# Performance work log

Hardware: AMD Instinct MI355X
Metric: run time of the kernel (lower is better)

## Reference

```python
import jax, jax.numpy as jnp
import numpy as np

WEIGHT_BIT = 8
ACT_BIT = 8
EPS = 1e-8

def ste_round(v):
    # straight-through estimator round (matches torch ste_round in QAT)
    return v + jax.lax.stop_gradient(jnp.round(v) - v)

def setup_inputs() -> dict:
    key = jax.random.key(0)
    k1, k2, k3, k4 = jax.random.split(key, 4)
    B, D_IN, D_OUT = 8192, 4096, 4096
    x = jax.random.normal(k1, (B, D_IN), dtype=jnp.float32)
    act_scaling_factor = jax.random.uniform(k2, (1,), dtype=jnp.float32, minval=0.01, maxval=0.05)
    W = jax.random.normal(k3, (D_OUT, D_IN), dtype=jnp.float32) * 0.02
    b = jax.random.normal(k4, (D_OUT,), dtype=jnp.float32) * 0.02
    return {"x": x, "act_scaling_factor": act_scaling_factor, "W": W, "b": b}

def reference(x, act_scaling_factor, W, b):
    n_w = 2 ** (WEIGHT_BIT - 1) - 1  # 127
    # ---- QuantLinear: symmetric per-channel weight quantization ----
    w_absmax = jnp.maximum(jnp.abs(W.min(axis=1)), jnp.abs(W.max(axis=1)))  # [out]
    fc_sf = jnp.maximum(w_absmax, EPS) / n_w  # weight scaling factor, [out]
    w_int = jnp.clip(ste_round(W / fc_sf[:, None]), -n_w - 1, n_w)
    bias_sf = fc_sf * act_scaling_factor  # [out] (act_sf is scalar-shaped [1])
    b_int = ste_round(b / bias_sf)
    x_int = x / act_scaling_factor
    out = (jnp.matmul(x_int, w_int.T) + b_int) * bias_sf  # [B, out]
    # ---- ReLU ----
    out = jax.nn.relu(out)
    # ---- QuantAct, asymmetric per-tensor requantization ----
    levels = 2 ** ACT_BIT - 1  # 255
    x_min = jnp.minimum(out.min(), 0.0)
    x_max = jnp.maximum(out.max(), 0.0)
    act_sf_new = jnp.maximum(x_max - x_min, EPS) / levels  # scalar
    zp = jnp.round(-x_min / act_sf_new)
    x_q = jnp.clip(ste_round(out / act_sf_new) + zp, 0.0, float(levels))
    x_out = (x_q - zp) * act_sf_new
    return (x_out, fc_sf, jnp.reshape(act_sf_new, (1,)))
```

## Files before the change

kernel.cpp:

```cpp
#include <hip/hip_runtime.h>
#include <hip/hip_bf16.h>
#include <stdint.h>

#define B_DIM 8192
#define IN_DIM 4096
#define OUT_DIM 4096

typedef __attribute__((ext_vector_type(8))) short s16x8;
typedef __attribute__((ext_vector_type(4))) float f32x4;

__device__ __forceinline__ unsigned short f2bf_rn(float f) {
    unsigned int u = __float_as_uint(f);
    u = (u + 0x7FFFu + ((u >> 16) & 1u)) >> 16;
    return (unsigned short)u;
}

__device__ __forceinline__ void async16(unsigned short* l, const unsigned short* g) {
    __builtin_amdgcn_global_load_lds(
        (const __attribute__((address_space(1))) void*)g,
        (__attribute__((address_space(3))) void*)l, 16, 0, 0);
}

__global__ __launch_bounds__(256) void quant_w(
    const float* __restrict__ W, const float* __restrict__ b,
    const float* __restrict__ act_sf, unsigned short* __restrict__ wq,
    float* __restrict__ fc_sf_out, float* __restrict__ bb,
    float* __restrict__ gmax)
{
    int o = blockIdx.x;
    int t = threadIdx.x;
    const float4* Wr = (const float4*)(W + (size_t)o * IN_DIM);
    float4 v[4];
    float amax = 0.f;
#pragma unroll
    for (int j = 0; j < 4; ++j) {
        v[j] = Wr[t + j * 256];
        amax = fmaxf(amax, fmaxf(fmaxf(fabsf(v[j].x), fabsf(v[j].y)),
                                 fmaxf(fabsf(v[j].z), fabsf(v[j].w))));
    }
#pragma unroll
    for (int off = 32; off > 0; off >>= 1)
        amax = fmaxf(amax, __shfl_down(amax, off, 64));
    __shared__ float red[4];
    if ((t & 63) == 0) red[t >> 6] = amax;
    __syncthreads();
    float wmax = fmaxf(fmaxf(red[0], red[1]), fmaxf(red[2], red[3]));
    float sf = fmaxf(wmax, 1e-8f) / 127.0f;

    unsigned short* wr = wq + (size_t)o * IN_DIM;
#pragma unroll
    for (int j = 0; j < 4; ++j) {
        ushort4 q;
        q.x = f2bf_rn(fminf(fmaxf(rintf(v[j].x / sf), -128.f), 127.f));
        q.y = f2bf_rn(fminf(fmaxf(rintf(v[j].y / sf), -128.f), 127.f));
        q.z = f2bf_rn(fminf(fmaxf(rintf(v[j].z / sf), -128.f), 127.f));
        q.w = f2bf_rn(fminf(fmaxf(rintf(v[j].w / sf), -128.f), 127.f));
        ((ushort4*)wr)[t + j * 256] = q;
    }
    if (t == 0) {
        fc_sf_out[o] = sf;
        float bsf = sf * act_sf[0];
        float bi = rintf(b[o] / bsf);
        bb[o] = bi * bsf;
        if (o == 0) gmax[0] = 0.f;
    }
}

__global__ __launch_bounds__(256) void cvt_x(const float* __restrict__ x,
                                             unsigned short* __restrict__ xq)
{
    size_t i = ((size_t)blockIdx.x * 256 + threadIdx.x) * 8;
#pragma unroll
    for (int j = 0; j < 2; ++j) {
        float4 v = *(const float4*)(x + i + j * 4);
        ushort4 q;
        q.x = f2bf_rn(v.x); q.y = f2bf_rn(v.y);
        q.z = f2bf_rn(v.z); q.w = f2bf_rn(v.w);
        *(ushort4*)(xq + i + j * 4) = q;
    }
}

__global__ __launch_bounds__(256) void gemm_bt(
    const unsigned short* __restrict__ A, const unsigned short* __restrict__ Bw,
    const float* __restrict__ fc_sf, const float* __restrict__ bb,
    float* __restrict__ C, float* __restrict__ gmax)
{
    __shared__ unsigned short sA[128 * 32];
    __shared__ unsigned short sB[128 * 32];
    __shared__ float redm[4];

    int t = threadIdx.x;
    int bn = blockIdx.x & 31;
    int bm = blockIdx.x >> 5;
    int lane = t & 63;
    int w = t >> 6;
    int quad = lane >> 4;
    int l16 = lane & 15;
    int m0 = bm * 128, n0 = bn * 128;
    int wm = (w & 1) * 64, wn = (w >> 1) * 64;

    int r0 = t >> 2;
    int gc = (t & 3) ^ ((r0 & 3) ^ ((r0 >> 2) & 1));
    const unsigned short* gA0 = A + (size_t)(m0 + r0) * IN_DIM + gc * 8;
    const unsigned short* gA1 = A + (size_t)(m0 + 64 + r0) * IN_DIM + gc * 8;
    const unsigned short* gB0 = Bw + (size_t)(n0 + r0) * IN_DIM + gc * 8;
    const unsigned short* gB1 = Bw + (size_t)(n0 + 64 + r0) * IN_DIM + gc * 8;
    unsigned short* lA0 = sA + t * 8;
    unsigned short* lA1 = sA + (t + 256) * 8;
    unsigned short* lB0 = sB + t * 8;
    unsigned short* lB1 = sB + (t + 256) * 8;

    int swzl = (l16 & 3) ^ ((l16 >> 2) & 1);
    const unsigned short* pa = sA + (wm + l16) * 32 + ((quad ^ swzl) * 8);
    const unsigned short* pb = sB + (wn + l16) * 32 + ((quad ^ swzl) * 8);

    f32x4 acc[4][4];
#pragma unroll
    for (int mi = 0; mi < 4; ++mi)
#pragma unroll
        for (int ni = 0; ni < 4; ++ni)
            acc[mi][ni] = (f32x4){0.f, 0.f, 0.f, 0.f};

    for (int kk = 0; kk < IN_DIM; kk += 32) {
        __syncthreads();
        async16(lA0, gA0 + kk);
        async16(lA1, gA1 + kk);
        async16(lB0, gB0 + kk);
        async16(lB1, gB1 + kk);
        asm volatile("s_waitcnt vmcnt(0)" ::: "memory");
        __syncthreads();

        s16x8 af[4], bf[4];
#pragma unroll
        for (int i = 0; i < 4; ++i) af[i] = *(const s16x8*)(pa + i * 16 * 32);
#pragma unroll
        for (int i = 0; i < 4; ++i) bf[i] = *(const s16x8*)(pb + i * 16 * 32);
#pragma unroll
        for (int mi = 0; mi < 4; ++mi)
#pragma unroll
            for (int ni = 0; ni < 4; ++ni)
                acc[mi][ni] = __builtin_amdgcn_mfma_f32_16x16x32_bf16(
                    af[mi], bf[ni], acc[mi][ni], 0, 0, 0);
    }

    float tmax = 0.f;
#pragma unroll
    for (int ni = 0; ni < 4; ++ni) {
        int col = n0 + wn + ni * 16 + l16;
        float s = fc_sf[col];
        float bbv = bb[col];
#pragma unroll
        for (int mi = 0; mi < 4; ++mi) {
            int rowb = m0 + wm + mi * 16 + quad * 4;
#pragma unroll
            for (int r = 0; r < 4; ++r) {
                float vv = acc[mi][ni][r] * s + bbv;
                vv = fmaxf(vv, 0.f);
                tmax = fmaxf(tmax, vv);
                C[(size_t)(rowb + r) * OUT_DIM + col] = vv;
            }
        }
    }
#pragma unroll
    for (int off = 32; off > 0; off >>= 1)
        tmax = fmaxf(tmax, __shfl_down(tmax, off, 64));
    if (lane == 0) redm[w] = tmax;
    __syncthreads();
    if (t == 0) {
        float bmax = fmaxf(fmaxf(redm[0], redm[1]), fmaxf(redm[2], redm[3]));
        atomicMax((int*)gmax, __float_as_int(bmax));
    }
}

__global__ __launch_bounds__(256) void requant(float* __restrict__ C,
    const float* __restrict__ gmax, float* __restrict__ sf_out)
{
    float sf = fmaxf(gmax[0], 1e-8f) / 255.0f;
    size_t i = ((size_t)blockIdx.x * 256 + threadIdx.x) * 8;
#pragma unroll
    for (int j = 0; j < 2; ++j) {
        float4 v = *(const float4*)(C + i + j * 4);
        v.x = fminf(rintf(v.x / sf), 255.f) * sf;
        v.y = fminf(rintf(v.y / sf), 255.f) * sf;
        v.z = fminf(rintf(v.z / sf), 255.f) * sf;
        v.w = fminf(rintf(v.w / sf), 255.f) * sf;
        *(float4*)(C + i + j * 4) = v;
    }
    if (i == 0) sf_out[0] = sf;
}

extern "C" void kernel_launch(void* const* d_in, const int* in_sizes, int n_in,
                              void* d_out, int out_size, void* d_ws, size_t ws_size,
                              hipStream_t stream)
{
    const float* x      = (const float*)d_in[0];
    const float* act_sf = (const float*)d_in[1];
    const float* W      = (const float*)d_in[2];
    const float* b      = (const float*)d_in[3];

    float* out        = (float*)d_out;
    float* fc_sf_out  = out + (size_t)B_DIM * OUT_DIM;
    float* act_sf_out = fc_sf_out + OUT_DIM;

    char* ws = (char*)d_ws;
    float* bb   = (float*)ws;
    float* gmax = (float*)(ws + 16384);
    unsigned short* xq = (unsigned short*)(ws + 32768);
    unsigned short* wq = xq + (size_t)B_DIM * IN_DIM;

    quant_w<<<OUT_DIM, 256, 0, stream>>>(W, b, act_sf, wq, fc_sf_out, bb, gmax);
    cvt_x<<<(B_DIM * IN_DIM) / 2048, 256, 0, stream>>>(x, xq);
    gemm_bt<<<(B_DIM / 128) * (OUT_DIM / 128), 256, 0, stream>>>(
        xq, wq, fc_sf_out, bb, out, gmax);
    requant<<<(B_DIM * OUT_DIM) / 2048, 256, 0, stream>>>(out, gmax, act_sf_out);
}
```

Before: 639.9 us.

## Double GEMM K-tile to 64, merge prep kernels, widen requant per-thread work

The GEMM K-step grows from 32 to 64, with an 8-way XOR swizzle for the wider LDS rows, so each barrier pair now feeds 32 MFMAs instead of 16. The weight quantization and x-to-bf16 conversion kernels become one launch that branches on block index. The requant kernel now processes 16 floats per thread with half as many blocks. This cuts sync overhead and launch count in exchange for twice the LDS per block, which may lower occupancy, and there is still no double buffering.

Result: no change. 632.2 us (-1.2%).

```diff
diff --git a/kernel.cpp b/kernel.cpp
--- a/kernel.cpp
+++ b/kernel.cpp
@@ -21,62 +21,61 @@
         (__attribute__((address_space(3))) void*)l, 16, 0, 0);
 }
 
-__global__ __launch_bounds__(256) void quant_w(
+__global__ __launch_bounds__(256) void prep(
     const float* __restrict__ W, const float* __restrict__ b,
-    const float* __restrict__ act_sf, unsigned short* __restrict__ wq,
+    const float* __restrict__ act_sf, const float* __restrict__ x,
+    unsigned short* __restrict__ wq, unsigned short* __restrict__ xq,
     float* __restrict__ fc_sf_out, float* __restrict__ bb,
     float* __restrict__ gmax)
 {
-    int o = blockIdx.x;
+    __shared__ float red[4];
     int t = threadIdx.x;
-    const float4* Wr = (const float4*)(W + (size_t)o * IN_DIM);
-    float4 v[4];
-    float amax = 0.f;
-#pragma unroll
-    for (int j = 0; j < 4; ++j) {
-        v[j] = Wr[t + j * 256];
-        amax = fmaxf(amax, fmaxf(fmaxf(fabsf(v[j].x), fabsf(v[j].y)),
-                                 fmaxf(fabsf(v[j].z), fabsf(v[j].w))));
-    }
-#pragma unroll
-    for (int off = 32; off > 0; off >>= 1)
-        amax = fmaxf(amax, __shfl_down(amax, off, 64));
-    __shared__ float red[4];
-    if ((t & 63) == 0) red[t >> 6] = amax;
-    __syncthreads();
-    float wmax = fmaxf(fmaxf(red[0], red[1]), fmaxf(red[2], red[3]));
-    float sf = fmaxf(wmax, 1e-8f) / 127.0f;
-
-    unsigned short* wr = wq + (size_t)o * IN_DIM;
-#pragma unroll
-    for (int j = 0; j < 4; ++j) {
-        ushort4 q;
-        q.x = f2bf_rn(fminf(fmaxf(rintf(v[j].x / sf), -128.f), 127.f));
-        q.y = f2bf_rn(fminf(fmaxf(rintf(v[j].y / sf), -128.f), 127.f));
-        q.z = f2bf_rn(fminf(fmaxf(rintf(v[j].z / sf), -128.f), 127.f));
-        q.w = f2bf_rn(fminf(fmaxf(rintf(v[j].w / sf), -128.f), 127.f));
-        ((ushort4*)wr)[t + j * 256] = q;
-    }
-    if (t == 0) {
-        fc_sf_out[o] = sf;
-        float bsf = sf * act_sf[0];
-        float bi = rintf(b[o] / bsf);
-        bb[o] = bi * bsf;
-        if (o == 0) gmax[0] = 0.f;
-    }
-}
-
-__global__ __launch_bounds__(256) void cvt_x(const float* __restrict__ x,
-                                             unsigned short* __restrict__ xq)
-{
-    size_t i = ((size_t)blockIdx.x * 256 + threadIdx.x) * 8;
-#pragma unroll
-    for (int j = 0; j < 2; ++j) {
-        float4 v = *(const float4*)(x + i + j * 4);
-        ushort4 q;
-        q.x = f2bf_rn(v.x); q.y = f2bf_rn(v.y);
-        q.z = f2bf_rn(v.z); q.w = f2bf_rn(v.w);
-        *(ushort4*)(xq + i + j * 4) = q;
+    if (blockIdx.x < OUT_DIM) {
+        int o = blockIdx.x;
+        const float4* Wr = (const float4*)(W + (size_t)o * IN_DIM);
+        float4 v[4];
+        float amax = 0.f;
+#pragma unroll
+        for (int j = 0; j < 4; ++j) {
+            v[j] = Wr[t + j * 256];
+            amax = fmaxf(amax, fmaxf(fmaxf(fabsf(v[j].x), fabsf(v[j].y)),
+                                     fmaxf(fabsf(v[j].z), fabsf(v[j].w))));
+        }
+#pragma unroll
+        for (int off = 32; off > 0; off >>= 1)
+            amax = fmaxf(amax, __shfl_down(amax, off, 64));
+        if ((t & 63) == 0) red[t >> 6] = amax;
+        __syncthreads();
+        float wmax = fmaxf(fmaxf(red[0], red[1]), fmaxf(red[2], red[3]));
+        float sf = fmaxf(wmax, 1e-8f) / 127.0f;
+
+        unsigned short* wr = wq + (size_t)o * IN_DIM;
+#pragma unroll
+        for (int j = 0; j < 4; ++j) {
+            ushort4 q;
+            q.x = f2bf_rn(fminf(fmaxf(rintf(v[j].x / sf), -128.f), 127.f));
+            q.y = f2bf_rn(fminf(fmaxf(rintf(v[j].y / sf), -128.f), 127.f));
+            q.z = f2bf_rn(fminf(fmaxf(rintf(v[j].z / sf), -128.f), 127.f));
+            q.w = f2bf_rn(fminf(fmaxf(rintf(v[j].w / sf), -128.f), 127.f));
+            ((ushort4*)wr)[t + j * 256] = q;
+        }
+        if (t == 0) {
+            fc_sf_out[o] = sf;
+            float bsf = sf * act_sf[0];
+            float bi = rintf(b[o] / bsf);
+            bb[o] = bi * bsf;
+            if (o == 0) gmax[0] = 0.f;
+        }
+    } else {
+        size_t i = ((size_t)(blockIdx.x - OUT_DIM) * 256 + t) * 8;
+#pragma unroll
+        for (int j = 0; j < 2; ++j) {
+            float4 v = *(const float4*)(x + i + j * 4);
+            ushort4 q;
+            q.x = f2bf_rn(v.x); q.y = f2bf_rn(v.y);
+            q.z = f2bf_rn(v.z); q.w = f2bf_rn(v.w);
+            *(ushort4*)(xq + i + j * 4) = q;
+        }
     }
 }
 
@@ -85,8 +84,8 @@
     const float* __restrict__ fc_sf, const float* __restrict__ bb,
     float* __restrict__ C, float* __restrict__ gmax)
 {
-    __shared__ unsigned short sA[128 * 32];
-    __shared__ unsigned short sB[128 * 32];
+    __shared__ unsigned short sA[128 * 64];
+    __shared__ unsigned short sB[128 * 64];
     __shared__ float redm[4];
 
     int t = threadIdx.x;
@@ -99,20 +98,28 @@
     int m0 = bm * 128, n0 = bn * 128;
     int wm = (w & 1) * 64, wn = (w >> 1) * 64;
 
-    int r0 = t >> 2;
-    int gc = (t & 3) ^ ((r0 & 3) ^ ((r0 >> 2) & 1));
-    const unsigned short* gA0 = A + (size_t)(m0 + r0) * IN_DIM + gc * 8;
-    const unsigned short* gA1 = A + (size_t)(m0 + 64 + r0) * IN_DIM + gc * 8;
-    const unsigned short* gB0 = Bw + (size_t)(n0 + r0) * IN_DIM + gc * 8;
-    const unsigned short* gB1 = Bw + (size_t)(n0 + 64 + r0) * IN_DIM + gc * 8;
-    unsigned short* lA0 = sA + t * 8;
-    unsigned short* lA1 = sA + (t + 256) * 8;
-    unsigned short* lB0 = sB + t * 8;
-    unsigned short* lB1 = sB + (t + 256) * 8;
-
-    int swzl = (l16 & 3) ^ ((l16 >> 2) & 1);
-    const unsigned short* pa = sA + (wm + l16) * 32 + ((quad ^ swzl) * 8);
-    const unsigned short* pb = sB + (wn + l16) * 32 + ((quad ^ swzl) * 8);
+    int r0 = t >> 3;
+    int gc = (t & 7) ^ (r0 & 7);
+    const unsigned short* gA[4];
+    const unsigned short* gB[4];
+    unsigned short* lA[4];
+    unsigned short* lB[4];
+#pragma unroll
+    for (int j = 0; j < 4; ++j) {
+        gA[j] = A + (size_t)(m0 + j * 32 + r0) * IN_DIM + gc * 8;
+        gB[j] = Bw + (size_t)(n0 + j * 32 + r0) * IN_DIM + gc * 8;
+        lA[j] = sA + (j * 256 + t) * 8;
+        lB[j] = sB + (j * 256 + t) * 8;
+    }
+
+    int swzl = l16 & 7;
+    const unsigned short* pa[2];
+    const unsigned short* pb[2];
+#pragma unroll
+    for (int h = 0; h < 2; ++h) {
+        pa[h] = sA + (wm + l16) * 64 + ((4 * h + quad) ^ swzl) * 8;
+        pb[h] = sB + (wn + l16) * 64 + ((4 * h + quad) ^ swzl) * 8;
+    }
 
     f32x4 acc[4][4];
 #pragma unroll
@@ -121,26 +128,30 @@
         for (int ni = 0; ni < 4; ++ni)
             acc[mi][ni] = (f32x4){0.f, 0.f, 0.f, 0.f};
 
-    for (int kk = 0; kk < IN_DIM; kk += 32) {
+    for (int kk = 0; kk < IN_DIM; kk += 64) {
         __syncthreads();
-        async16(lA0, gA0 + kk);
-        async16(lA1, gA1 + kk);
-        async16(lB0, gB0 + kk);
-        async16(lB1, gB1 + kk);
+#pragma unroll
+        for (int j = 0; j < 4; ++j) {
+            async16(lA[j], gA[j] + kk);
+            async16(lB[j], gB[j] + kk);
+        }
         asm volatile("s_waitcnt vmcnt(0)" ::: "memory");
         __syncthreads();
 
-        s16x8 af[4], bf[4];
-#pragma unroll
-        for (int i = 0; i < 4; ++i) af[i] = *(const s16x8*)(pa + i * 16 * 32);
-#pragma unroll
-        for (int i = 0; i < 4; ++i) bf[i] = *(const s16x8*)(pb + i * 16 * 32);
-#pragma unroll
-        for (int mi = 0; mi < 4; ++mi)
-#pragma unroll
-            for (int ni = 0; ni < 4; ++ni)
-                acc[mi][ni] = __builtin_amdgcn_mfma_f32_16x16x32_bf16(
-                    af[mi], bf[ni], acc[mi][ni], 0, 0, 0);
+#pragma unroll
+        for (int h = 0; h < 2; ++h) {
+            s16x8 af[4], bf[4];
+#pragma unroll
+            for (int i = 0; i < 4; ++i) af[i] = *(const s16x8*)(pa[h] + i * 16 * 64);
+#pragma unroll
+            for (int i = 0; i < 4; ++i) bf[i] = *(const s16x8*)(pb[h] + i * 16 * 64);
+#pragma unroll
+            for (int mi = 0; mi < 4; ++mi)
+#pragma unroll
+                for (int ni = 0; ni < 4; ++ni)
+                    acc[mi][ni] = __builtin_amdgcn_mfma_f32_16x16x32_bf16(
+                        af[mi], bf[ni], acc[mi][ni], 0, 0, 0);
+        }
     }
 
     float tmax = 0.f;
@@ -176,9 +187,9 @@
     const float* __restrict__ gmax, float* __restrict__ sf_out)
 {
     float sf = fmaxf(gmax[0], 1e-8f) / 255.0f;
-    size_t i = ((size_t)blockIdx.x * 256 + threadIdx.x) * 8;
-#pragma unroll
-    for (int j = 0; j < 2; ++j) {
+    size_t i = ((size_t)blockIdx.x * 256 + threadIdx.x) * 16;
+#pragma unroll
+    for (int j = 0; j < 4; ++j) {
         float4 v = *(const float4*)(C + i + j * 4);
         v.x = fminf(rintf(v.x / sf), 255.f) * sf;
         v.y = fminf(rintf(v.y / sf), 255.f) * sf;
@@ -208,9 +219,9 @@
     unsigned short* xq = (unsigned short*)(ws + 32768);
     unsigned short* wq = xq + (size_t)B_DIM * IN_DIM;
 
-    quant_w<<<OUT_DIM, 256, 0, stream>>>(W, b, act_sf, wq, fc_sf_out, bb, gmax);
-    cvt_x<<<(B_DIM * IN_DIM) / 2048, 256, 0, stream>>>(x, xq);
+    prep<<<OUT_DIM + (B_DIM * IN_DIM) / 2048, 256, 0, stream>>>(
+        W, b, act_sf, x, wq, xq, fc_sf_out, bb, gmax);
     gemm_bt<<<(B_DIM / 128) * (OUT_DIM / 128), 256, 0, stream>>>(
         xq, wq, fc_sf_out, bb, out, gmax);
-    requant<<<(B_DIM * OUT_DIM) / 2048, 256, 0, stream>>>(out, gmax, act_sf_out);
-}
+    requant<<<(B_DIM * OUT_DIM) / 4096, 256, 0, stream>>>(out, gmax, act_sf_out);
+}
```
